# Kernel tuning notes

Measured on AMD Instinct MI355X. Metric: run time of the kernel, lower is better.

Reference implementation:

```python
import jax, jax.numpy as jnp
import numpy as np

TEMPERATURE = 0.07

def _l2_normalize(x):
    # F.normalize(x, dim=1): x / max(||x||, eps)
    n = jnp.linalg.norm(x, axis=1, keepdims=True)
    return x / jnp.maximum(n, 1e-12)

def setup_inputs() -> dict:
    key = jax.random.key(0)
    k1, k2, k3, k4 = jax.random.split(key, 4)
    B, D, N = 4096, 256, 131072
    anchor = jax.random.normal(k1, (B, D), dtype=jnp.float32)
    positive = jax.random.normal(k2, (B, D), dtype=jnp.float32)
    negatives = jax.random.normal(k3, (N, D), dtype=jnp.float32)
    neg_batch_indices = jnp.sort(jax.random.randint(k4, (N,), 0, B, dtype=jnp.int32))
    return {"anchor": anchor, "positive": positive, "negatives": negatives,
            "neg_batch_indices": neg_batch_indices}

def reference(anchor, positive, negatives, neg_batch_indices):
    B = anchor.shape[0]
    a = _l2_normalize(anchor)            # [B, D]
    p = _l2_normalize(positive)          # [B, D]
    n = _l2_normalize(negatives)         # [N, D]
    pos_sim = jnp.sum(a * p, axis=1) / TEMPERATURE                     # [B]
    # only sims between a negative and its owning anchor are ever used ->
    # gather instead of the dense [B, N] matmul the torch loop masks.
    neg_sim = jnp.sum(a[neg_batch_indices] * n, axis=1) / TEMPERATURE  # [N]
    seg_max = jax.ops.segment_max(neg_sim, neg_batch_indices, num_segments=B)  # -inf for empty
    counts = jax.ops.segment_sum(jnp.ones_like(neg_sim), neg_batch_indices, num_segments=B)
    m = jax.lax.stop_gradient(jnp.maximum(pos_sim, seg_max))           # [B], finite
    sum_exp = jnp.exp(pos_sim - m) + jax.ops.segment_sum(
        jnp.exp(neg_sim - m[neg_batch_indices]), neg_batch_indices, num_segments=B)
    loss_i = -pos_sim + m + jnp.log(sum_exp)                           # [B]
    loss_i = jnp.where(counts > 0, loss_i, 0.0)  # torch skips empty groups
    loss = jnp.sum(loss_i) / B
    correct = (counts > 0) & (pos_sim > seg_max)  # (pos > all negs), empty -> skipped
    accuracy = jnp.mean(correct.astype(jnp.float32))
    return loss, accuracy
```

## Files before the change

kernel.cpp:

```cpp
#include <hip/hip_runtime.h>
#include <math.h>

#define TEMP_INV (1.0f / 0.07f)

typedef float vf4 __attribute__((ext_vector_type(4)));

#define DOT4(a, n) ((a).x*(n).x + (a).y*(n).y + (a).z*(n).z + (a).w*(n).w)

__device__ __forceinline__ float wave_reduce_sum(float v) {
    #pragma unroll
    for (int off = 32; off; off >>= 1) v += __shfl_down(v, off);
    return v;
}

__device__ __forceinline__ float wave_reduce_max(float v) {
    #pragma unroll
    for (int off = 32; off; off >>= 1) v = fmaxf(v, __shfl_down(v, off));
    return v;
}

__device__ __forceinline__ float merge2(float lo, float hi, int span, int lane) {
    float a = lo + __shfl_xor(lo, span);
    float b = hi + __shfl_xor(hi, span);
    return (lane & span) ? b : a;
}

__global__ __launch_bounds__(256, 8)
void k_main(const float* __restrict__ A, const float* __restrict__ P,
            const float* __restrict__ Ng, const int* __restrict__ idx,
            float* __restrict__ inv_na, float* __restrict__ pos_sim,
            float* __restrict__ raw, int* __restrict__ seg_start,
            int B, int N) {
    const int bid  = (int)blockIdx.x;
    const int wib  = threadIdx.x >> 6;
    const int lane = threadIdx.x & 63;
    const int wave = bid * 4 + wib;
    const int nwaves = (int)gridDim.x * 4;

    if (wave < B) {
        int b = wave;
        const float4 a = reinterpret_cast<const float4*>(A + (size_t)b * 256)[lane];
        const float4 p = reinterpret_cast<const float4*>(P + (size_t)b * 256)[lane];
        float sa = DOT4(a, a);
        float sp = DOT4(p, p);
        float dq = DOT4(a, p);
        sa = wave_reduce_sum(sa);
        sp = wave_reduce_sum(sp);
        dq = wave_reduce_sum(dq);
        if (lane == 0) {
            float ia = 1.0f / fmaxf(sqrtf(sa), 1e-12f);
            float ip = 1.0f / fmaxf(sqrtf(sp), 1e-12f);
            inv_na[b]  = ia;
            pos_sim[b] = dq * ia * ip * TEMP_INV;
        }
    }

    {
        int t = bid * 256 + (int)threadIdx.x;
        int stride = (int)gridDim.x * 256;
        for (int j = t; j <= N; j += stride) {
            if (j == 0) {
                int c = idx[0];
                for (int v = 0; v <= c; ++v) seg_start[v] = 0;
            } else if (j < N) {
                int prev = idx[j - 1], cur = idx[j];
                for (int v = prev + 1; v <= cur; ++v) seg_start[v] = j;
            } else {
                int prev = idx[N - 1];
                for (int v = prev + 1; v <= B; ++v) seg_start[v] = N;
            }
        }
    }

    const int nchunks = N >> 2;
    const float4* A4 = reinterpret_cast<const float4*>(A);
    const vf4* N4 = reinterpret_cast<const vf4*>(Ng);
    for (int chunk = wave; chunk < nchunks; chunk += nwaves) {
        int j0 = chunk << 2;
        int4 bi = *reinterpret_cast<const int4*>(idx + j0);
        int b0 = __builtin_amdgcn_readfirstlane(bi.x);
        int b1 = __builtin_amdgcn_readfirstlane(bi.y);
        int b2 = __builtin_amdgcn_readfirstlane(bi.z);
        int b3 = __builtin_amdgcn_readfirstlane(bi.w);

        const vf4 n0 = N4[(size_t)(j0 + 0) * 64 + lane];
        const vf4 n1 = N4[(size_t)(j0 + 1) * 64 + lane];
        const vf4 n2 = N4[(size_t)(j0 + 2) * 64 + lane];
        const vf4 n3 = N4[(size_t)(j0 + 3) * 64 + lane];

        const float4 a0 = A4[(size_t)b0 * 64 + lane];
        const float4 a1 = A4[(size_t)b1 * 64 + lane];
        const float4 a2 = A4[(size_t)b2 * 64 + lane];
        const float4 a3 = A4[(size_t)b3 * 64 + lane];

        float sn0 = DOT4(n0, n0);
        float dp0 = DOT4(a0, n0);
        float sn1 = DOT4(n1, n1);
        float dp1 = DOT4(a1, n1);
        float sn2 = DOT4(n2, n2);
        float dp2 = DOT4(a2, n2);
        float sn3 = DOT4(n3, n3);
        float dp3 = DOT4(a3, n3);

        float nv0 = merge2(sn0, sn2, 32, lane);
        float nv1 = merge2(dp0, dp2, 32, lane);
        float nv2 = merge2(sn1, sn3, 32, lane);
        float nv3 = merge2(dp1, dp3, 32, lane);
        float m0  = merge2(nv0, nv2, 16, lane);
        float m1  = merge2(nv1, nv3, 16, lane);
        float f   = merge2(m0,  m1,   8, lane);
        f += __shfl_xor(f, 4);
        f += __shfl_xor(f, 2);
        f += __shfl_xor(f, 1);

        float fdp = __shfl_down(f, 8);
        if ((lane & 15) == 0) {
            int r = lane >> 4;
            raw[j0 + r] = fdp * (1.0f / fmaxf(sqrtf(f), 1e-12f)) * TEMP_INV;
        }
    }
}

__global__ void k_seg(const float* __restrict__ raw, const int* __restrict__ seg_start,
                      const float* __restrict__ inv_na, const float* __restrict__ pos_sim,
                      float* __restrict__ loss_i, float* __restrict__ corr, int B) {
    int b = (int)blockIdx.x * 4 + (threadIdx.x >> 6);
    int lane = threadIdx.x & 63;
    if (b >= B) return;

    int s = seg_start[b];
    int e = seg_start[b + 1];

    float ps = pos_sim[b];
    float ia = inv_na[b];

    float l_val = 0.0f, c_val = 0.0f;
    if (e > s) {
        const float M = TEMP_INV;
        float mx = -INFINITY, se = 0.0f;
        for (int j = s + lane; j < e; j += 64) {
            float t = raw[j] * ia;
            mx = fmaxf(mx, t);
            se += expf(t - M);
        }
        mx = wave_reduce_max(mx);
        se = wave_reduce_sum(se);
        mx = __shfl(mx, 0);
        se = __shfl(se, 0);
        l_val = -ps + M + logf(se + expf(ps - M));
        c_val = (ps > mx) ? 1.0f : 0.0f;
    }
    if (lane == 0) { loss_i[b] = l_val; corr[b] = c_val; }
}

__global__ __launch_bounds__(1024)
void k_final(const float* __restrict__ loss_i, const float* __restrict__ corr,
             float* __restrict__ out, int B) {
    __shared__ float sl[16];
    __shared__ float sc[16];
    int tid = (int)threadIdx.x, lane = tid & 63, wid = tid >> 6;
    float l = 0.0f, c = 0.0f;
    for (int i = tid; i < B; i += 1024) { l += loss_i[i]; c += corr[i]; }
    l = wave_reduce_sum(l);
    c = wave_reduce_sum(c);
    if (lane == 0) { sl[wid] = l; sc[wid] = c; }
    __syncthreads();
    if (wid == 0) {
        float lv = (lane < 16) ? sl[lane] : 0.0f;
        float cv = (lane < 16) ? sc[lane] : 0.0f;
        lv = wave_reduce_sum(lv);
        cv = wave_reduce_sum(cv);
        if (lane == 0) {
            out[0] = lv / (float)B;
            out[1] = cv / (float)B;
        }
    }
}

extern "C" void kernel_launch(void* const* d_in, const int* in_sizes, int n_in,
                              void* d_out, int out_size, void* d_ws, size_t ws_size,
                              hipStream_t stream) {
    const float* anchor    = (const float*)d_in[0];
    const float* positive  = (const float*)d_in[1];
    const float* negatives = (const float*)d_in[2];
    const int*   idx       = (const int*)d_in[3];

    const int D = 256;
    const int B = in_sizes[0] / D;
    const int N = in_sizes[2] / D;

    float* ws        = (float*)d_ws;
    float* raw       = ws;
    float* inv_na    = ws + N;
    float* pos_sim   = ws + N + B;
    float* loss_i    = ws + N + 2 * B;
    float* corr      = ws + N + 3 * B;
    int*   seg_start = (int*)(ws + N + 4 * B);

    float* out = (float*)d_out;

    k_main<<<2048, 256, 0, stream>>>(anchor, positive, negatives, idx,
                                     inv_na, pos_sim, raw, seg_start, B, N);

    k_seg<<<(B + 3) / 4, 256, 0, stream>>>(raw, seg_start, inv_na, pos_sim,
                                           loss_i, corr, B);

    k_final<<<1, 1024, 0, stream>>>(loss_i, corr, out, B);
}
```

Measured before the change: 34.39 us.

## Fuse similarity and segment reduction into one per-anchor kernel with binary search

Merges the negative-similarity kernel and the segment softmax kernel into a single kernel where each wave owns one anchor. The wave finds its segment bounds with a 64-way ballot search over the sorted indices, keeps the anchor row in registers, and reduces max and exp-sum on the fly. This drops the intermediate raw similarity buffer, the seg_start construction and one launch. The cost is load imbalance across segments of uneven length, partial wasted loads on segment tails, and serial search latency at the start of each wave.

```diff
diff --git a/kernel.cpp b/kernel.cpp
--- a/kernel.cpp
+++ b/kernel.cpp
@@ -25,82 +25,64 @@
     return (lane & span) ? b : a;
 }
 
-__global__ __launch_bounds__(256, 8)
-void k_main(const float* __restrict__ A, const float* __restrict__ P,
-            const float* __restrict__ Ng, const int* __restrict__ idx,
-            float* __restrict__ inv_na, float* __restrict__ pos_sim,
-            float* __restrict__ raw, int* __restrict__ seg_start,
-            int B, int N) {
-    const int bid  = (int)blockIdx.x;
-    const int wib  = threadIdx.x >> 6;
+__device__ __forceinline__ int wave_lb(const int* __restrict__ idx, int N,
+                                       int target, int lane) {
+    int lo = 0, hi = N;
+    while (hi > lo) {
+        int R = hi - lo;
+        int step = (R + 62) / 63;
+        int pos = lo + lane * step;
+        int v = (pos < N) ? idx[pos] : 0x7fffffff;
+        unsigned long long m = __ballot(v < target);
+        int p = __popcll(m);
+        int nlo = (p > 0) ? (lo + (p - 1) * step + 1) : lo;
+        int nhi = (p < 64) ? min(hi, min(lo + p * step, N)) : hi;
+        lo = nlo; hi = nhi;
+    }
+    return lo;
+}
+
+__global__ void k_fused(const float* __restrict__ A, const float* __restrict__ P,
+                        const float* __restrict__ Ng, const int* __restrict__ idx,
+                        float* __restrict__ loss_i, float* __restrict__ corr,
+                        int B, int N) {
     const int lane = threadIdx.x & 63;
-    const int wave = bid * 4 + wib;
-    const int nwaves = (int)gridDim.x * 4;
+    const int b = (int)blockIdx.x * 4 + (int)(threadIdx.x >> 6);
+    if (b >= B) return;
 
-    if (wave < B) {
-        int b = wave;
-        const float4 a = reinterpret_cast<const float4*>(A + (size_t)b * 256)[lane];
-        const float4 p = reinterpret_cast<const float4*>(P + (size_t)b * 256)[lane];
-        float sa = DOT4(a, a);
-        float sp = DOT4(p, p);
-        float dq = DOT4(a, p);
-        sa = wave_reduce_sum(sa);
-        sp = wave_reduce_sum(sp);
-        dq = wave_reduce_sum(dq);
-        if (lane == 0) {
-            float ia = 1.0f / fmaxf(sqrtf(sa), 1e-12f);
-            float ip = 1.0f / fmaxf(sqrtf(sp), 1e-12f);
-            inv_na[b]  = ia;
-            pos_sim[b] = dq * ia * ip * TEMP_INV;
-        }
+    int s = wave_lb(idx, N, b, lane);
+    int e = wave_lb(idx, N, b + 1, lane);
+
+    const float4 a  = reinterpret_cast<const float4*>(A)[(size_t)b * 64 + lane];
+    const float4 pv = reinterpret_cast<const float4*>(P)[(size_t)b * 64 + lane];
+    float sa = DOT4(a, a);
+    float sp = DOT4(pv, pv);
+    float dq = DOT4(a, pv);
+    sa = wave_reduce_sum(sa);
+    sp = wave_reduce_sum(sp);
+    dq = wave_reduce_sum(dq);
+    float ia = 0.0f, ps = 0.0f;
+    if (lane == 0) {
+        ia = 1.0f / fmaxf(sqrtf(sa), 1e-12f);
+        float ip = 1.0f / fmaxf(sqrtf(sp), 1e-12f);
+        ps = dq * ia * ip * TEMP_INV;
     }
+    ia = __shfl(ia, 0);
+    ps = __shfl(ps, 0);
 
-    {
-        int t = bid * 256 + (int)threadIdx.x;
-        int stride = (int)gridDim.x * 256;
-        for (int j = t; j <= N; j += stride) {
-            if (j == 0) {
-                int c = idx[0];
-                for (int v = 0; v <= c; ++v) seg_start[v] = 0;
-            } else if (j < N) {
-                int prev = idx[j - 1], cur = idx[j];
-                for (int v = prev + 1; v <= cur; ++v) seg_start[v] = j;
-            } else {
-                int prev = idx[N - 1];
-                for (int v = prev + 1; v <= B; ++v) seg_start[v] = N;
-            }
-        }
-    }
+    const vf4* N4 = reinterpret_cast<const vf4*>(Ng);
+    float mxa = -INFINITY, sea = 0.0f;
+    for (int j = s; j < e; j += 4) {
+        vf4 n0 = {0.f, 0.f, 0.f, 0.f}, n1 = n0, n2 = n0, n3 = n0;
+        n0 = N4[(size_t)j * 64 + lane];
+        if (j + 1 < e) n1 = N4[(size_t)(j + 1) * 64 + lane];
+        if (j + 2 < e) n2 = N4[(size_t)(j + 2) * 64 + lane];
+        if (j + 3 < e) n3 = N4[(size_t)(j + 3) * 64 + lane];
 
-    const int nchunks = N >> 2;
-    const float4* A4 = reinterpret_cast<const float4*>(A);
-    const vf4* N4 = reinterpret_cast<const vf4*>(Ng);
-    for (int chunk = wave; chunk < nchunks; chunk += nwaves) {
-        int j0 = chunk << 2;
-        int4 bi = *reinterpret_cast<const int4*>(idx + j0);
-        int b0 = __builtin_amdgcn_readfirstlane(bi.x);
-        int b1 = __builtin_amdgcn_readfirstlane(bi.y);
-        int b2 = __builtin_amdgcn_readfirstlane(bi.z);
-        int b3 = __builtin_amdgcn_readfirstlane(bi.w);
-
-        const vf4 n0 = N4[(size_t)(j0 + 0) * 64 + lane];
-        const vf4 n1 = N4[(size_t)(j0 + 1) * 64 + lane];
-        const vf4 n2 = N4[(size_t)(j0 + 2) * 64 + lane];
-        const vf4 n3 = N4[(size_t)(j0 + 3) * 64 + lane];
-
-        const float4 a0 = A4[(size_t)b0 * 64 + lane];
-        const float4 a1 = A4[(size_t)b1 * 64 + lane];
-        const float4 a2 = A4[(size_t)b2 * 64 + lane];
-        const float4 a3 = A4[(size_t)b3 * 64 + lane];
-
-        float sn0 = DOT4(n0, n0);
-        float dp0 = DOT4(a0, n0);
-        float sn1 = DOT4(n1, n1);
-        float dp1 = DOT4(a1, n1);
-        float sn2 = DOT4(n2, n2);
-        float dp2 = DOT4(a2, n2);
-        float sn3 = DOT4(n3, n3);
-        float dp3 = DOT4(a3, n3);
+        float sn0 = DOT4(n0, n0), dp0 = DOT4(a, n0);
+        float sn1 = DOT4(n1, n1), dp1 = DOT4(a, n1);
+        float sn2 = DOT4(n2, n2), dp2 = DOT4(a, n2);
+        float sn3 = DOT4(n3, n3), dp3 = DOT4(a, n3);
 
         float nv0 = merge2(sn0, sn2, 32, lane);
         float nv1 = merge2(dp0, dp2, 32, lane);
@@ -116,41 +98,25 @@
         float fdp = __shfl_down(f, 8);
         if ((lane & 15) == 0) {
             int r = lane >> 4;
-            raw[j0 + r] = fdp * (1.0f / fmaxf(sqrtf(f), 1e-12f)) * TEMP_INV;
+            if (j + r < e) {
+                float t = fdp * (1.0f / fmaxf(sqrtf(f), 1e-12f)) * ia * TEMP_INV;
+                mxa = fmaxf(mxa, t);
+                sea += expf(t - TEMP_INV);
+            }
         }
     }
-}
 
-__global__ void k_seg(const float* __restrict__ raw, const int* __restrict__ seg_start,
-                      const float* __restrict__ inv_na, const float* __restrict__ pos_sim,
-                      float* __restrict__ loss_i, float* __restrict__ corr, int B) {
-    int b = (int)blockIdx.x * 4 + (threadIdx.x >> 6);
-    int lane = threadIdx.x & 63;
-    if (b >= B) return;
-
-    int s = seg_start[b];
-    int e = seg_start[b + 1];
-
-    float ps = pos_sim[b];
-    float ia = inv_na[b];
-
-    float l_val = 0.0f, c_val = 0.0f;
-    if (e > s) {
-        const float M = TEMP_INV;
-        float mx = -INFINITY, se = 0.0f;
-        for (int j = s + lane; j < e; j += 64) {
-            float t = raw[j] * ia;
-            mx = fmaxf(mx, t);
-            se += expf(t - M);
+    float mx = wave_reduce_max(mxa);
+    float se = wave_reduce_sum(sea);
+    if (lane == 0) {
+        float l = 0.0f, c = 0.0f;
+        if (e > s) {
+            l = -ps + TEMP_INV + logf(se + expf(ps - TEMP_INV));
+            c = (ps > mx) ? 1.0f : 0.0f;
         }
-        mx = wave_reduce_max(mx);
-        se = wave_reduce_sum(se);
-        mx = __shfl(mx, 0);
-        se = __shfl(se, 0);
-        l_val = -ps + M + logf(se + expf(ps - M));
-        c_val = (ps > mx) ? 1.0f : 0.0f;
+        loss_i[b] = l;
+        corr[b]   = c;
     }
-    if (lane == 0) { loss_i[b] = l_val; corr[b] = c_val; }
 }
 
 __global__ __launch_bounds__(1024)
@@ -189,21 +155,14 @@
     const int B = in_sizes[0] / D;
     const int N = in_sizes[2] / D;
 
-    float* ws        = (float*)d_ws;
-    float* raw       = ws;
-    float* inv_na    = ws + N;
-    float* pos_sim   = ws + N + B;
-    float* loss_i    = ws + N + 2 * B;
-    float* corr      = ws + N + 3 * B;
-    int*   seg_start = (int*)(ws + N + 4 * B);
+    float* ws     = (float*)d_ws;
+    float* loss_i = ws;
+    float* corr   = ws + B;
 
     float* out = (float*)d_out;
 
-    k_main<<<2048, 256, 0, stream>>>(anchor, positive, negatives, idx,
-                                     inv_na, pos_sim, raw, seg_start, B, N);
-
-    k_seg<<<(B + 3) / 4, 256, 0, stream>>>(raw, seg_start, inv_na, pos_sim,
-                                           loss_i, corr, B);
+    k_fused<<<(B + 3) / 4, 256, 0, stream>>>(anchor, positive, negatives, idx,
+                                             loss_i, corr, B, N);
 
     k_final<<<1, 1024, 0, stream>>>(loss_i, corr, out, B);
 }
```

Measured after the change: 34.79 us. No clear change (+1.2%).
